# Optimization experiments

Hardware: AMD Instinct MI355X
Metric: run time of the kernel (lower is better)

The kernel has to match this reference:

```python
import jax, jax.numpy as jnp
import numpy as np

DEGREE = 3
NUM_POINTS = 1024
EPS = 1e-5


def jacobi_kan(x, coeffs, a=1.0, b=1.0, degree=DEGREE):
    # x: (B, C_in, N) -> y: (B, C_out, N)
    t = jnp.tanh(jnp.transpose(x, (0, 2, 1)))  # (B, N, C_in)
    polys = [jnp.ones_like(t)]
    if degree > 0:
        polys.append((a - b + (a + b + 2.0) * t) / 2.0)
    for i in range(2, degree + 1):
        A = (2 * i + a + b - 1) * (2 * i + a + b) / (2 * i * (i + a + b))
        B = (2 * i + a + b - 1) * (a ** 2 - b ** 2) / (2 * i * (i + a + b) * (2 * i + a + b - 2))
        C = -2 * (i + a - 1) * (i + b - 1) * (2 * i + a + b) / (2 * i * (i + a + b) * (2 * i + a + b - 2))
        polys.append((A * t + B) * polys[-1] + C * polys[-2])
    jac = jnp.stack(polys, axis=-1)  # (B, N, C_in, D+1)
    return jnp.einsum('bnid,iod->bon', jac, coeffs)


def batchnorm(x):
    # x: (B, C, N); training-mode BN with batch stats, gamma=1, beta=0
    m = jnp.mean(x, axis=(0, 2), keepdims=True)
    v = jnp.var(x, axis=(0, 2), keepdims=True)
    return (x - m) * jax.lax.rsqrt(v + EPS)


def setup_inputs() -> dict:
    key = jax.random.key(0)
    ks = jax.random.split(key, 11)
    dims = [(2, 64), (64, 64), (64, 64), (64, 128), (128, 1024),
            (1088, 512), (512, 256), (256, 128), (128, 128), (128, 3)]
    inp = {"x": jax.random.normal(ks[0], (32, 2, NUM_POINTS), dtype=jnp.float32)}
    for idx, (i, o) in enumerate(dims):
        std = 1.0 / (i * (DEGREE + 1))
        inp[f"w{idx+1}"] = std * jax.random.normal(ks[idx + 1], (i, o, DEGREE + 1), dtype=jnp.float32)
    return inp


def reference(x, w1, w2, w3, w4, w5, w6, w7, w8, w9, w10):
    h = batchnorm(jacobi_kan(x, w1))
    h = batchnorm(jacobi_kan(h, w2))
    local_feature = h                                  # (B, 64, N)
    h = batchnorm(jacobi_kan(h, w3))
    h = batchnorm(jacobi_kan(h, w4))
    h = batchnorm(jacobi_kan(h, w5))                   # (B, 1024, N)
    gf = jnp.max(h, axis=2, keepdims=True)             # (B, 1024, 1)
    gf = jnp.broadcast_to(gf, (h.shape[0], h.shape[1], NUM_POINTS))
    h = jnp.concatenate([local_feature, gf], axis=1)   # (B, 1088, N)
    h = batchnorm(jacobi_kan(h, w6))
    h = batchnorm(jacobi_kan(h, w7))
    h = batchnorm(jacobi_kan(h, w8))
    h = batchnorm(jacobi_kan(h, w9))
    return jacobi_kan(h, w10)                          # (B, 3, N)
```

## Files before the change

kernel.cpp:

```cpp
#include <hip/hip_runtime.h>

#define BATCH 32
#define NPTS  1024
#define NTOT  (BATCH * NPTS)

typedef _Float16 half8  __attribute__((ext_vector_type(8)));
typedef _Float16 half2v __attribute__((ext_vector_type(2)));
typedef float    f32x4  __attribute__((ext_vector_type(4)));


__device__ __forceinline__ float fast_tanh(float x) {
  float ax = fabsf(x);
  float e  = __expf(-2.0f * ax);
  float t  = (1.0f - e) / (1.0f + e);
  return x < 0.0f ? -t : t;
}

__device__ __forceinline__ void jacobi4(float t, float& p0, float& p1, float& p2, float& p3) {
  float t2 = t * t;
  p0 = 1.0f;
  p1 = 2.0f * t;
  p2 = 3.75f * t2 - 0.75f;
  p3 = t * (7.0f * t2 - 3.0f);
}

__device__ __forceinline__ unsigned encf(float f) {
  unsigned b = __float_as_uint(f);
  return b ^ ((unsigned)((int)b >> 31) | 0x80000000u);
}
__device__ __forceinline__ float decf(unsigned u) {
  unsigned b = (u & 0x80000000u) ? (u ^ 0x80000000u) : ~u;
  return __uint_as_float(b);
}

__global__ void zero_ws(unsigned* __restrict__ p, int n) {
  int i = blockIdx.x * 256 + threadIdx.x;
  if (i < n) p[i] = 0u;
}

__global__ void conv_w16(const float* __restrict__ w, half8* __restrict__ wh,
                         int C_in, int C_out, int BN) {
  const int nslot = C_in >> 1;
  int tid = blockIdx.x * 256 + threadIdx.x;
  int oL = tid % BN;
  int r  = tid / BN;
  int s  = r % nslot;
  int ot = r / nslot;
  int i  = s << 1;
  int o  = ot * BN + oL;
  const float4 wa = *(const float4*)(w + (((size_t)i * C_out + o) << 2));
  const float4 wb = *(const float4*)(w + (((size_t)(i + 1) * C_out + o) << 2));
  half8 h;
  h[0] = (_Float16)(wa.x * 64.0f); h[1] = (_Float16)(wa.y * 64.0f);
  h[2] = (_Float16)(wa.z * 64.0f); h[3] = (_Float16)(wa.w * 64.0f);
  h[4] = (_Float16)(wb.x * 64.0f); h[5] = (_Float16)(wb.y * 64.0f);
  h[6] = (_Float16)(wb.z * 64.0f); h[7] = (_Float16)(wb.w * 64.0f);
  wh[tid] = h;
}

__global__ __launch_bounds__(256) void act_tanh16(
    const float* __restrict__ y, const float2* __restrict__ st,
    unsigned* __restrict__ T16, int C)
{
  const int nslot = C >> 1;
  const int b  = blockIdx.x / nslot;
  const int s  = blockIdx.x - b * nslot;
  const int n  = threadIdx.x << 2;
  const float* yp = y + (((size_t)(b * C + (s << 1))) << 10) + n;
  const float2 s0 = st[(s << 1)];
  const float2 s1 = st[(s << 1) + 1];
  float4 v0 = *(const float4*)yp;
  float4 v1 = *(const float4*)(yp + 1024);
  float a0[4] = {v0.x, v0.y, v0.z, v0.w};
  float a1[4] = {v1.x, v1.y, v1.z, v1.w};
  unsigned r[4];
#pragma unroll
  for (int k = 0; k < 4; ++k) {
    _Float16 h0 = (_Float16)fast_tanh((a0[k] - s0.x) * s0.y);
    _Float16 h1 = (_Float16)fast_tanh((a1[k] - s1.x) * s1.y);
    unsigned lo = (unsigned)__builtin_bit_cast(unsigned short, h0);
    unsigned hi = (unsigned)__builtin_bit_cast(unsigned short, h1);
    r[k] = lo | (hi << 16);
  }
  *(uint4*)(T16 + (((size_t)(b * nslot + s)) << 10) + n) = make_uint4(r[0], r[1], r[2], r[3]);
}

template<int NBW>
__global__ __launch_bounds__(NBW * 128, 2) void kan_mfma7(
    const unsigned* __restrict__ T16,
    const half8* __restrict__ wh,
    const float* __restrict__ bias,
    float*       __restrict__ out,
    float2*      __restrict__ spart,
    float*       __restrict__ stat_acc,
    unsigned*    __restrict__ max_acc,
    int C_in, int C_out)
{
  constexpr int BN = NBW * 64;
  const int nslot = C_in >> 1;
  __shared__ float sredS[BN][2], sredS2[BN][2], sredM[BN][2];

  const int t    = threadIdx.x;
  const int lane = t & 63;
  const int col  = lane & 15;
  const int quad = lane >> 4;
  const int wv   = t >> 6;
  const int wm   = wv & 1;
  const int wn   = wv >> 1;
  const int b    = blockIdx.x >> 3;
  const int n0   = (blockIdx.x & 7) << 7;
  const int o0   = blockIdx.y * BN;

  f32x4 acc[4][4];
#pragma unroll
  for (int i = 0; i < 4; ++i)
#pragma unroll
    for (int j = 0; j < 4; ++j)
#pragma unroll
      for (int k = 0; k < 4; ++k) acc[i][j][k] = 0.0f;

  const unsigned* Tp = T16 + (((size_t)(b * nslot + quad)) << 10) + n0 + (wm << 6) + col;
  const half8*    Bp = wh + (size_t)blockIdx.y * nslot * BN + (size_t)quad * BN + wn * 64 + col;

  const half2v c375  = {(_Float16)3.75f,  (_Float16)3.75f};
  const half2v cm075 = {(_Float16)-0.75f, (_Float16)-0.75f};
  const half2v c70   = {(_Float16)7.0f,   (_Float16)7.0f};
  const half2v cm30  = {(_Float16)-3.0f,  (_Float16)-3.0f};

#define KLOAD(TTR, BFR, J) do {                                            \
    const unsigned* tp_ = Tp + (((size_t)(unsigned)(J)) << 12);            \
    const half8*    bp_ = Bp + (size_t)(unsigned)(J) * (BN << 2);          \
    TTR[0] = tp_[0];  TTR[1] = tp_[16];                                    \
    TTR[2] = tp_[32]; TTR[3] = tp_[48];                                    \
    BFR[0] = bp_[0];  BFR[1] = bp_[16];                                    \
    BFR[2] = bp_[32]; BFR[3] = bp_[48];                                    \
  } while (0)

#define KSTEP(TTR, BFR) do {                                               \
    half8 af_[4];                                                          \
    _Pragma("unroll")                                                      \
    for (int fm_ = 0; fm_ < 4; ++fm_) {                                    \
      half2v tt = __builtin_bit_cast(half2v, TTR[fm_]);                    \
      half2v t2 = tt * tt;                                                 \
      half2v q1 = tt + tt;                                                 \
      half2v q2 = t2 * c375 + cm075;                                       \
      half2v q3 = tt * (t2 * c70 + cm30);                                  \
      half8 h;                                                             \
      h[0] = (_Float16)1.0f; h[1] = q1[0]; h[2] = q2[0]; h[3] = q3[0];     \
      h[4] = (_Float16)1.0f; h[5] = q1[1]; h[6] = q2[1]; h[7] = q3[1];     \
      af_[fm_] = h;                                                        \
    }                                                                      \
    _Pragma("unroll")                                                      \
    for (int fm_ = 0; fm_ < 4; ++fm_) {                                    \
      _Pragma("unroll")                                                    \
      for (int fn_ = 0; fn_ < 4; ++fn_)                                    \
        acc[fm_][fn_] = __builtin_amdgcn_mfma_f32_16x16x32_f16(            \
            af_[fm_], BFR[fn_], acc[fm_][fn_], 0, 0, 0);                   \
    }                                                                      \
  } while (0)

  const int nIt = nslot >> 2;
  unsigned ttA[4], ttB[4];
  half8    bfA[4], bfB[4];
  KLOAD(ttA, bfA, 0);
  KLOAD(ttB, bfB, 1);
  int it = 0;
  for (; it + 3 < nIt; it += 2) {
    KSTEP(ttA, bfA); KLOAD(ttA, bfA, it + 2);
    KSTEP(ttB, bfB); KLOAD(ttB, bfB, it + 3);
  }
  KSTEP(ttA, bfA);
  KSTEP(ttB, bfB);

#undef KLOAD
#undef KSTEP

  const float inv64 = 0.015625f;
#pragma unroll
  for (int fn = 0; fn < 4; ++fn) {
    const int cl = (wn << 6) + (fn << 4) + col;
    const int o  = o0 + cl;
    const float bb = bias ? bias[b * C_out + o] : 0.0f;
    float s = 0.f, s2 = 0.f, mx = -3.4e38f;
#pragma unroll
    for (int fm = 0; fm < 4; ++fm) {
      float v0 = acc[fm][fn][0] * inv64 + bb;
      float v1 = acc[fm][fn][1] * inv64 + bb;
      float v2 = acc[fm][fn][2] * inv64 + bb;
      float v3 = acc[fm][fn][3] * inv64 + bb;
      if (out) {
        *(float4*)(out + (((size_t)(b * C_out + o)) << 10) + n0 + (wm << 6) + (fm << 4) + (quad << 2)) =
            make_float4(v0, v1, v2, v3);
      }
      s  += v0 + v1 + v2 + v3;
      s2 += v0 * v0 + v1 * v1 + v2 * v2 + v3 * v3;
      mx  = fmaxf(fmaxf(v0, v1), fmaxf(fmaxf(v2, v3), mx));
    }
    s  += __shfl_down(s, 32);  s  += __shfl_down(s, 16);
    s2 += __shfl_down(s2, 32); s2 += __shfl_down(s2, 16);
    mx  = fmaxf(mx, __shfl_down(mx, 32)); mx = fmaxf(mx, __shfl_down(mx, 16));
    if (lane < 16) {
      sredS [cl][wm] = s;
      sredS2[cl][wm] = s2;
      sredM [cl][wm] = mx;
    }
  }
  __syncthreads();
  if (t < BN) {
    const int o = o0 + t;
    float s  = sredS [t][0] + sredS [t][1];
    float s2 = sredS2[t][0] + sredS2[t][1];
    if (out) {
      spart[(o << 8) + blockIdx.x] = make_float2(s, s2);
    } else {
      float mx = fmaxf(sredM[t][0], sredM[t][1]);
      atomicAdd(&stat_acc[o], s);
      atomicAdd(&stat_acc[C_out + o], s2);
      atomicMax(&max_acc[b * C_out + o], encf(mx));
    }
  }
}

template<int BM, int BN>
__global__ __launch_bounds__(256) void kan_gemm(
    const float*  __restrict__ in, const float2* __restrict__ stats,
    const float*  __restrict__ w, float* __restrict__ out,
    float2* __restrict__ spart, int C_in, int C_out)
{
  static_assert(BM * BN == 256 * 64, "8x8-per-thread tile requires BM*BN == 16384");
  constexpr int TM = BM / 8;
  constexpr int AE = 8 * BM / 256;
  constexpr int BE = 8 * BN / 256;
  __shared__ __align__(16) float As[32][BM];
  __shared__ __align__(16) float Bs[32][BN];

  const int t  = threadIdx.x;
  const int tpb = NPTS / BM;
  const int b  = blockIdx.x / tpb;
  const int n0 = (blockIdx.x % tpb) * BM;
  const int o0 = blockIdx.y * BN;
  const int tm = t % TM;
  const int to = t / TM;

  float acc[2][4][2][4];
#pragma unroll
  for (int a = 0; a < 2; ++a)
#pragma unroll
    for (int c = 0; c < 4; ++c)
#pragma unroll
      for (int d = 0; d < 2; ++d)
#pragma unroll
        for (int e = 0; e < 4; ++e) acc[a][c][d][e] = 0.0f;

  const int nch = (C_in + 7) >> 3;
  for (int ch = 0; ch < nch; ++ch) {
    const int i0 = ch << 3;
    __syncthreads();
#pragma unroll
    for (int r = 0; r < AE; ++r) {
      int e  = t + (r << 8);
      int il = e / BM, n = e % BM;
      int i  = i0 + il;
      float p0 = 0.f, p1 = 0.f, p2 = 0.f, p3 = 0.f;
      if (i < C_in) {
        float v = in[((size_t)(b * C_in + i) << 10) + n0 + n];
        if (stats) { float2 s = stats[i]; v = (v - s.x) * s.y; }
        jacobi4(fast_tanh(v), p0, p1, p2, p3);
      }
      As[(il << 2) + 0][n] = p0;
      As[(il << 2) + 1][n] = p1;
      As[(il << 2) + 2][n] = p2;
      As[(il << 2) + 3][n] = p3;
    }
#pragma unroll
    for (int r = 0; r < BE; ++r) {
      int e  = t + (r << 8);
      int il = e / BN, o = e % BN;
      int i  = i0 + il;
      float4 wv = make_float4(0.f, 0.f, 0.f, 0.f);
      if (i < C_in) wv = *(const float4*)(w + (((size_t)i * C_out + o0 + o) << 2));
      Bs[(il << 2) + 0][o] = wv.x;
      Bs[(il << 2) + 1][o] = wv.y;
      Bs[(il << 2) + 2][o] = wv.z;
      Bs[(il << 2) + 3][o] = wv.w;
    }
    __syncthreads();
#pragma unroll 8
    for (int k = 0; k < 32; ++k) {
      const float4 a0 = *(const float4*)&As[k][tm << 2];
      const float4 a1 = *(const float4*)&As[k][(BM / 2) + (tm << 2)];
      const float4 b0 = *(const float4*)&Bs[k][to << 2];
      const float4 b1 = *(const float4*)&Bs[k][(BN / 2) + (to << 2)];
      const float am[2][4] = {{a0.x, a0.y, a0.z, a0.w}, {a1.x, a1.y, a1.z, a1.w}};
      const float bo[2][4] = {{b0.x, b0.y, b0.z, b0.w}, {b1.x, b1.y, b1.z, b1.w}};
#pragma unroll
      for (int oh = 0; oh < 2; ++oh)
#pragma unroll
        for (int oj = 0; oj < 4; ++oj) {
          const float bv = bo[oh][oj];
#pragma unroll
          for (int mh = 0; mh < 2; ++mh)
#pragma unroll
            for (int mj = 0; mj < 4; ++mj)
              acc[oh][oj][mh][mj] = fmaf(bv, am[mh][mj], acc[oh][oj][mh][mj]);
        }
    }
  }

#pragma unroll
  for (int oh = 0; oh < 2; ++oh)
#pragma unroll
    for (int oj = 0; oj < 4; ++oj) {
      const int o = o0 + oh * (BN / 2) + (to << 2) + oj;
      float s = 0.f, s2 = 0.f;
#pragma unroll
      for (int mh = 0; mh < 2; ++mh) {
        float4 v = make_float4(acc[oh][oj][mh][0], acc[oh][oj][mh][1],
                               acc[oh][oj][mh][2], acc[oh][oj][mh][3]);
        *(float4*)(out + (((size_t)(b * C_out + o)) << 10) + n0 + mh * (BM / 2) + (tm << 2)) = v;
        s  += v.x + v.y + v.z + v.w;
        s2 += v.x * v.x + v.y * v.y + v.z * v.z + v.w * v.w;
      }
#pragma unroll
      for (int off = TM / 2; off > 0; off >>= 1) {
        s  += __shfl_down(s, off, TM);
        s2 += __shfl_down(s2, off, TM);
      }
      if (tm == 0) spart[(o << 8) + blockIdx.x] = make_float2(s, s2);
    }
}

__global__ __launch_bounds__(256) void bn_finalize2(
    const float2* __restrict__ spart, float2* __restrict__ stats, int C, int nxb)
{
  int c = blockIdx.x, t = threadIdx.x;
  float s = 0.f, s2 = 0.f;
  if (t < nxb) { float2 p = spart[(c << 8) + t]; s = p.x; s2 = p.y; }
#pragma unroll
  for (int off = 32; off > 0; off >>= 1) {
    s  += __shfl_down(s, off);
    s2 += __shfl_down(s2, off);
  }
  __shared__ float rs[4], rs2[4];
  int wid = t >> 6;
  if ((t & 63) == 0) { rs[wid] = s; rs2[wid] = s2; }
  __syncthreads();
  if (t == 0) {
    s  = rs[0] + rs[1] + rs[2] + rs[3];
    s2 = rs2[0] + rs2[1] + rs2[2] + rs2[3];
    float m   = s * (1.0f / NTOT);
    float var = s2 * (1.0f / NTOT) - m * m;
    stats[c] = make_float2(m, rsqrtf(var + 1e-5f));
  }
}

__global__ void bn_finalize(const float* __restrict__ stat_acc,
                            float2* __restrict__ stats, int C) {
  int c = blockIdx.x * 256 + threadIdx.x;
  if (c < C) {
    float m   = stat_acc[c] * (1.0f / NTOT);
    float var = stat_acc[C + c] * (1.0f / NTOT) - m * m;
    stats[c] = make_float2(m, rsqrtf(var + 1e-5f));
  }
}

__global__ __launch_bounds__(256) void pool_const6p(
    const unsigned* __restrict__ max_acc, const float2* __restrict__ stats5,
    const float* __restrict__ w6, float* __restrict__ cst)
{
  __shared__ __align__(16) float4 P[32][64];
  const int t  = threadIdx.x;
  const int ot = blockIdx.x;
  const int c0 = blockIdx.y << 6;
#pragma unroll
  for (int it = 0; it < 8; ++it) {
    int idx = t + (it << 8);
    int b = idx >> 6, cl = idx & 63;
    int c = c0 + cl;
    float mx = decf(max_acc[(b << 10) + c]);
    float2 s = stats5[c];
    float tt = fast_tanh((mx - s.x) * s.y);
    float p0, p1, p2, p3; jacobi4(tt, p0, p1, p2, p3);
    P[b][cl] = make_float4(p0, p1, p2, p3);
  }
  __syncthreads();
  const int oL = t & 63;
  const int bg = t >> 6;
  const int o  = (ot << 6) + oL;
  float acc[8];
#pragma unroll
  for (int i = 0; i < 8; ++i) acc[i] = 0.f;
  for (int cl = 0; cl < 64; ++cl) {
    const float4 wv = *(const float4*)(w6 + (((size_t)(64 + c0 + cl) * 512 + o) << 2));
#pragma unroll
    for (int bb = 0; bb < 8; ++bb) {
      float4 p = P[(bg << 3) + bb][cl];
      acc[bb] += p.x * wv.x + p.y * wv.y + p.z * wv.z + p.w * wv.w;
    }
  }
#pragma unroll
  for (int bb = 0; bb < 8; ++bb)
    atomicAdd(&cst[(((bg << 3) + bb) << 9) + o], acc[bb]);
}

__global__ __launch_bounds__(256) void kan_final(
    const float* __restrict__ in, const float2* __restrict__ stats,
    const float* __restrict__ w, float* __restrict__ out)
{
  int g = blockIdx.x * 256 + threadIdx.x;
  int b = g >> 10, n = g & 1023;
  float a0 = 0.f, a1 = 0.f, a2 = 0.f;
  for (int i = 0; i < 128; ++i) {
    float v = in[((size_t)(b * 128 + i) << 10) + n];
    float2 s = stats[i];
    float p0, p1, p2, p3; jacobi4(fast_tanh((v - s.x) * s.y), p0, p1, p2, p3);
    const float4 w0 = *(const float4*)(w + ((i * 3 + 0) << 2));
    const float4 w1 = *(const float4*)(w + ((i * 3 + 1) << 2));
    const float4 w2 = *(const float4*)(w + ((i * 3 + 2) << 2));
    a0 += p0 * w0.x + p1 * w0.y + p2 * w0.z + p3 * w0.w;
    a1 += p0 * w1.x + p1 * w1.y + p2 * w1.z + p3 * w1.w;
    a2 += p0 * w2.x + p1 * w2.y + p2 * w2.z + p3 * w2.w;
  }
  out[((b * 3 + 0) << 10) + n] = a0;
  out[((b * 3 + 1) << 10) + n] = a1;
  out[((b * 3 + 2) << 10) + n] = a2;
}

extern "C" void kernel_launch(void* const* d_in, const int* in_sizes, int n_in,
                              void* d_out, int out_size, void* d_ws, size_t ws_size,
                              hipStream_t stream) {
  const float* x   = (const float*)d_in[0];
  const float* w1  = (const float*)d_in[1];
  const float* w2  = (const float*)d_in[2];
  const float* w3  = (const float*)d_in[3];
  const float* w4  = (const float*)d_in[4];
  const float* w5  = (const float*)d_in[5];
  const float* w6  = (const float*)d_in[6];
  const float* w7  = (const float*)d_in[7];
  const float* w8  = (const float*)d_in[8];
  const float* w9  = (const float*)d_in[9];
  const float* w10 = (const float*)d_in[10];

  float* ws = (float*)d_ws;
  float*    stat_acc = ws + 0;
  unsigned* maxenc   = (unsigned*)(ws + 2048);
  float*    cst6     = ws + 34816;
  float2*   spart    = (float2*)(ws + 51200);
  float2*   stats1   = (float2*)(ws + 313344);
  float2*   stats2   = stats1 + 64;
  float2*   stats3   = stats2 + 64;
  float2*   stats4   = stats3 + 64;
  float2*   stats5   = stats4 + 128;
  float2*   stats6   = stats5 + 1024;
  float2*   stats7   = stats6 + 512;
  float2*   stats8   = stats7 + 256;
  float2*   stats9   = stats8 + 128;
  half8*    whbase = (half8*)(ws + 318464);
  half8*    h2 = whbase + 0;
  half8*    h3 = whbase + 2048;
  half8*    h4 = whbase + 4096;
  half8*    h5 = whbase + 8192;
  half8*    h6 = whbase + 73728;
  half8*    h7 = whbase + 90112;
  half8*    h8 = whbase + 155648;
  half8*    h9 = whbase + 172032;
  const size_t MF = 1048576;
  float*    P   = ws + MF;
  unsigned* T2  = (unsigned*)(P + 0 * MF);
  float*    y1  = P + 1 * MF;
  unsigned* T1  = (unsigned*)(P + 3 * MF);
  float*    y2  = P + 1 * MF;
  float*    y3  = P + 1 * MF;
  unsigned* T3  = (unsigned*)(P + 3 * MF);
  float*    y4  = P + 4 * MF;
  unsigned* T4  = (unsigned*)(P + 1 * MF);
  float*    y6  = P + 3 * MF;
  unsigned* T6  = (unsigned*)(P + 19 * MF);
  float*    y7  = P + 0 * MF;
  unsigned* T7  = (unsigned*)(P + 8 * MF);
  float*    y8  = P + 0 * MF;
  unsigned* T8  = (unsigned*)(P + 4 * MF);
  float*    y9  = P + 12 * MF;

  dim3 blk(256);
  zero_ws<<<200, blk, 0, stream>>>((unsigned*)ws, 51200);
  conv_w16<<<8,   blk, 0, stream>>>(w2, h2, 64, 64, 64);
  conv_w16<<<8,   blk, 0, stream>>>(w3, h3, 64, 64, 64);
  conv_w16<<<16,  blk, 0, stream>>>(w4, h4, 64, 128, 128);
  conv_w16<<<256, blk, 0, stream>>>(w5, h5, 128, 1024, 128);
  conv_w16<<<64,  blk, 0, stream>>>(w6, h6, 64, 512, 128);
  conv_w16<<<256, blk, 0, stream>>>(w7, h7, 512, 256, 128);
  conv_w16<<<64,  blk, 0, stream>>>(w8, h8, 256, 128, 128);
  conv_w16<<<32,  blk, 0, stream>>>(w9, h9, 128, 128, 128);

  kan_gemm<256, 64><<<dim3(128, 1), blk, 0, stream>>>(x, nullptr, w1, y1, spart, 2, 64);
  bn_finalize2<<<64, blk, 0, stream>>>(spart, stats1, 64, 128);
  act_tanh16<<<32 * 32, blk, 0, stream>>>(y1, stats1, T1, 64);
  kan_mfma7<1><<<dim3(256, 1), 128, 0, stream>>>(T1, h2, nullptr, y2, spart, nullptr, nullptr, 64, 64);
  bn_finalize2<<<64, blk, 0, stream>>>(spart, stats2, 64, 256);
  act_tanh16<<<32 * 32, blk, 0, stream>>>(y2, stats2, T2, 64);
  kan_mfma7<1><<<dim3(256, 1), 128, 0, stream>>>(T2, h3, nullptr, y3, spart, nullptr, nullptr, 64, 64);
  bn_finalize2<<<64, blk, 0, stream>>>(spart, stats3, 64, 256);
  act_tanh16<<<32 * 32, blk, 0, stream>>>(y3, stats3, T3, 64);
  kan_mfma7<2><<<dim3(256, 1), blk, 0, stream>>>(T3, h4, nullptr, y4, spart, nullptr, nullptr, 64, 128);
  bn_finalize2<<<128, blk, 0, stream>>>(spart, stats4, 128, 256);
  act_tanh16<<<32 * 64, blk, 0, stream>>>(y4, stats4, T4, 128);
  kan_mfma7<2><<<dim3(256, 8), blk, 0, stream>>>(T4, h5, nullptr, nullptr, nullptr, stat_acc, maxenc, 128, 1024);
  bn_finalize<<<4, blk, 0, stream>>>(stat_acc, stats5, 1024);
  pool_const6p<<<dim3(8, 16), blk, 0, stream>>>(maxenc, stats5, w6, cst6);
  kan_mfma7<2><<<dim3(256, 4), blk, 0, stream>>>(T2, h6, cst6, y6, spart, nullptr, nullptr, 64, 512);
  bn_finalize2<<<512, blk, 0, stream>>>(spart, stats6, 512, 256);
  act_tanh16<<<32 * 256, blk, 0, stream>>>(y6, stats6, T6, 512);
  kan_mfma7<2><<<dim3(256, 2), blk, 0, stream>>>(T6, h7, nullptr, y7, spart, nullptr, nullptr, 512, 256);
  bn_finalize2<<<256, blk, 0, stream>>>(spart, stats7, 256, 256);
  act_tanh16<<<32 * 128, blk, 0, stream>>>(y7, stats7, T7, 256);
  kan_mfma7<2><<<dim3(256, 1), blk, 0, stream>>>(T7, h8, nullptr, y8, spart, nullptr, nullptr, 256, 128);
  bn_finalize2<<<128, blk, 0, stream>>>(spart, stats8, 128, 256);
  act_tanh16<<<32 * 64, blk, 0, stream>>>(y8, stats8, T8, 128);
  kan_mfma7<2><<<dim3(256, 1), blk, 0, stream>>>(T8, h9, nullptr, y9, spart, nullptr, nullptr, 128, 128);
  bn_finalize2<<<128, blk, 0, stream>>>(spart, stats9, 128, 256);
  kan_final<<<128, blk, 0, stream>>>(y9, stats9, w10, (float*)d_out);
}
```

Baseline: 382.6 us.

## Drop constant P0 term from MFMA K dimension via precomputed weight row sums

Because the degree-0 Jacobi polynomial is always 1, its contribution is a per-output-channel sum of weights. The change precomputes that sum in a new kernel and adds it as a bias in the epilogue, so the MFMA loop only multiplies the three non-constant polynomial terms. Weights are repacked by degree (P1, P2, P3 groups of 8 input channels), which shrinks the GEMM K dimension by a quarter. In exchange the kernel holds more registers (16 T values and 12 B fragments per stage, double-buffered), which may cut occupancy, and it adds eight small launches.

```diff
diff --git a/kernel.cpp b/kernel.cpp
--- a/kernel.cpp
+++ b/kernel.cpp
@@ -38,24 +38,43 @@
   if (i < n) p[i] = 0u;
 }
 
-__global__ void conv_w16(const float* __restrict__ w, half8* __restrict__ wh,
-                         int C_in, int C_out, int BN) {
-  const int nslot = C_in >> 1;
+__global__ __launch_bounds__(256) void conv_w16p(
+    const float* __restrict__ w, half8* __restrict__ wh,
+    int C_in, int C_out, int BN)
+{
+  const int NS = C_in >> 5;
   int tid = blockIdx.x * 256 + threadIdx.x;
   int oL = tid % BN;
   int r  = tid / BN;
-  int s  = r % nslot;
-  int ot = r / nslot;
-  int i  = s << 1;
+  int pr = NS * 12;
+  int ot = r / pr;
+  int r2 = r - ot * pr;
+  int q  = r2 & 3;
+  int jj = (r2 >> 2) % 3;
+  int s  = (r2 >> 2) / 3;
   int o  = ot * BN + oL;
-  const float4 wa = *(const float4*)(w + (((size_t)i * C_out + o) << 2));
-  const float4 wb = *(const float4*)(w + (((size_t)(i + 1) * C_out + o) << 2));
+  int cb = (s << 5) + (q << 3);
   half8 h;
-  h[0] = (_Float16)(wa.x * 64.0f); h[1] = (_Float16)(wa.y * 64.0f);
-  h[2] = (_Float16)(wa.z * 64.0f); h[3] = (_Float16)(wa.w * 64.0f);
-  h[4] = (_Float16)(wb.x * 64.0f); h[5] = (_Float16)(wb.y * 64.0f);
-  h[6] = (_Float16)(wb.z * 64.0f); h[7] = (_Float16)(wb.w * 64.0f);
+#pragma unroll
+  for (int e = 0; e < 8; ++e) {
+    float v = w[(((size_t)(cb + e) * C_out + o) << 2) + (jj + 1)];
+    h[e] = (_Float16)(v * 64.0f);
+  }
   wh[tid] = h;
+}
+
+__global__ __launch_bounds__(256) void w0sum(
+    const float* __restrict__ w, float* __restrict__ s, int C_in, int C_out)
+{
+  __shared__ float r[3][64];
+  const int oL  = threadIdx.x & 63;
+  const int seg = threadIdx.x >> 6;
+  const int o   = (blockIdx.x << 6) + oL;
+  float a = 0.f;
+  for (int i = seg; i < C_in; i += 4) a += w[(((size_t)i * C_out + o) << 2)];
+  if (seg) r[seg - 1][oL] = a;
+  __syncthreads();
+  if (seg == 0) s[o] = a + r[0][oL] + r[1][oL] + r[2][oL];
 }
 
 __global__ __launch_bounds__(256) void act_tanh16(
@@ -86,9 +105,10 @@
 }
 
 template<int NBW>
-__global__ __launch_bounds__(NBW * 128, 2) void kan_mfma7(
+__global__ __launch_bounds__(NBW * 128, 2) void kan_mfma8(
     const unsigned* __restrict__ T16,
     const half8* __restrict__ wh,
+    const float* __restrict__ w0s,
     const float* __restrict__ bias,
     float*       __restrict__ out,
     float2*      __restrict__ spart,
@@ -98,6 +118,7 @@
 {
   constexpr int BN = NBW * 64;
   const int nslot = C_in >> 1;
+  const int NS    = C_in >> 5;
   __shared__ float sredS[BN][2], sredS2[BN][2], sredM[BN][2];
 
   const int t    = threadIdx.x;
@@ -119,53 +140,100 @@
 #pragma unroll
       for (int k = 0; k < 4; ++k) acc[i][j][k] = 0.0f;
 
-  const unsigned* Tp = T16 + (((size_t)(b * nslot + quad)) << 10) + n0 + (wm << 6) + col;
-  const half8*    Bp = wh + (size_t)blockIdx.y * nslot * BN + (size_t)quad * BN + wn * 64 + col;
+  const unsigned* Tp = T16 + (((size_t)(b * nslot + (quad << 2))) << 10) + n0 + (wm << 6) + col;
+  const half8*    Bp = wh + ((size_t)blockIdx.y * NS * 12 + quad) * BN + wn * 64 + col;
 
   const half2v c375  = {(_Float16)3.75f,  (_Float16)3.75f};
   const half2v cm075 = {(_Float16)-0.75f, (_Float16)-0.75f};
   const half2v c70   = {(_Float16)7.0f,   (_Float16)7.0f};
   const half2v cm30  = {(_Float16)-3.0f,  (_Float16)-3.0f};
 
-#define KLOAD(TTR, BFR, J) do {                                            \
-    const unsigned* tp_ = Tp + (((size_t)(unsigned)(J)) << 12);            \
-    const half8*    bp_ = Bp + (size_t)(unsigned)(J) * (BN << 2);          \
-    TTR[0] = tp_[0];  TTR[1] = tp_[16];                                    \
-    TTR[2] = tp_[32]; TTR[3] = tp_[48];                                    \
-    BFR[0] = bp_[0];  BFR[1] = bp_[16];                                    \
-    BFR[2] = bp_[32]; BFR[3] = bp_[48];                                    \
-  } while (0)
-
-#define KSTEP(TTR, BFR) do {                                               \
-    half8 af_[4];                                                          \
+#define KLOAD(TT, BF, S) do {                                              \
     _Pragma("unroll")                                                      \
-    for (int fm_ = 0; fm_ < 4; ++fm_) {                                    \
-      half2v tt = __builtin_bit_cast(half2v, TTR[fm_]);                    \
-      half2v t2 = tt * tt;                                                 \
-      half2v q1 = tt + tt;                                                 \
-      half2v q2 = t2 * c375 + cm075;                                       \
-      half2v q3 = tt * (t2 * c70 + cm30);                                  \
-      half8 h;                                                             \
-      h[0] = (_Float16)1.0f; h[1] = q1[0]; h[2] = q2[0]; h[3] = q3[0];     \
-      h[4] = (_Float16)1.0f; h[5] = q1[1]; h[6] = q2[1]; h[7] = q3[1];     \
-      af_[fm_] = h;                                                        \
+    for (int f_ = 0; f_ < 4; ++f_) {                                       \
+      _Pragma("unroll")                                                    \
+      for (int r_ = 0; r_ < 4; ++r_)                                       \
+        TT[f_ * 4 + r_] = Tp[(((size_t)(unsigned)((S) * 16 + r_)) << 10) + (f_ << 4)]; \
     }                                                                      \
     _Pragma("unroll")                                                      \
-    for (int fm_ = 0; fm_ < 4; ++fm_) {                                    \
+    for (int j_ = 0; j_ < 3; ++j_) {                                       \
       _Pragma("unroll")                                                    \
       for (int fn_ = 0; fn_ < 4; ++fn_)                                    \
-        acc[fm_][fn_] = __builtin_amdgcn_mfma_f32_16x16x32_f16(            \
-            af_[fm_], BFR[fn_], acc[fm_][fn_], 0, 0, 0);                   \
+        BF[j_ * 4 + fn_] = Bp[(size_t)(unsigned)((S) * 12 + j_ * 4) * BN + (fn_ << 4)]; \
     }                                                                      \
   } while (0)
 
-  const int nIt = nslot >> 2;
-  unsigned ttA[4], ttB[4];
-  half8    bfA[4], bfB[4];
+#define KSTEP(TT, BF) do {                                                 \
+    {                                                \
+      half8 ap_[4];                                                        \
+      _Pragma("unroll")                                                    \
+      for (int f_ = 0; f_ < 4; ++f_) {                                     \
+        unsigned u_[4];                                                    \
+        _Pragma("unroll")                                                  \
+        for (int r_ = 0; r_ < 4; ++r_) {                                   \
+          half2v tt = __builtin_bit_cast(half2v, TT[f_ * 4 + r_]);         \
+          u_[r_] = __builtin_bit_cast(unsigned, (half2v)(tt + tt));        \
+        }                                                                  \
+        ap_[f_] = __builtin_bit_cast(half8, make_uint4(u_[0], u_[1], u_[2], u_[3])); \
+      }                                                                    \
+      _Pragma("unroll")                                                    \
+      for (int fm_ = 0; fm_ < 4; ++fm_) {                                  \
+        _Pragma("unroll")                                                  \
+        for (int fn_ = 0; fn_ < 4; ++fn_)                                  \
+          acc[fm_][fn_] = __builtin_amdgcn_mfma_f32_16x16x32_f16(          \
+              ap_[fm_], BF[fn_], acc[fm_][fn_], 0, 0, 0);                  \
+      }                                                                    \
+    }                                                                      \
+    {                                    \
+      half8 ap_[4];                                                        \
+      _Pragma("unroll")                                                    \
+      for (int f_ = 0; f_ < 4; ++f_) {                                     \
+        unsigned u_[4];                                                    \
+        _Pragma("unroll")                                                  \
+        for (int r_ = 0; r_ < 4; ++r_) {                                   \
+          half2v tt = __builtin_bit_cast(half2v, TT[f_ * 4 + r_]);         \
+          half2v t2 = tt * tt;                                             \
+          u_[r_] = __builtin_bit_cast(unsigned, (half2v)(t2 * c375 + cm075)); \
+        }                                                                  \
+        ap_[f_] = __builtin_bit_cast(half8, make_uint4(u_[0], u_[1], u_[2], u_[3])); \
+      }                                                                    \
+      _Pragma("unroll")                                                    \
+      for (int fm_ = 0; fm_ < 4; ++fm_) {                                  \
+        _Pragma("unroll")                                                  \
+        for (int fn_ = 0; fn_ < 4; ++fn_)                                  \
+          acc[fm_][fn_] = __builtin_amdgcn_mfma_f32_16x16x32_f16(          \
+              ap_[fm_], BF[4 + fn_], acc[fm_][fn_], 0, 0, 0);              \
+      }                                                                    \
+    }                                                                      \
+    {                                       \
+      half8 ap_[4];                                                        \
+      _Pragma("unroll")                                                    \
+      for (int f_ = 0; f_ < 4; ++f_) {                                     \
+        unsigned u_[4];                                                    \
+        _Pragma("unroll")                                                  \
+        for (int r_ = 0; r_ < 4; ++r_) {                                   \
+          half2v tt = __builtin_bit_cast(half2v, TT[f_ * 4 + r_]);         \
+          half2v t2 = tt * tt;                                             \
+          u_[r_] = __builtin_bit_cast(unsigned, (half2v)(tt * (t2 * c70 + cm30))); \
+        }                                                                  \
+        ap_[f_] = __builtin_bit_cast(half8, make_uint4(u_[0], u_[1], u_[2], u_[3])); \
+      }                                                                    \
+      _Pragma("unroll")                                                    \
+      for (int fm_ = 0; fm_ < 4; ++fm_) {                                  \
+        _Pragma("unroll")                                                  \
+        for (int fn_ = 0; fn_ < 4; ++fn_)                                  \
+          acc[fm_][fn_] = __builtin_amdgcn_mfma_f32_16x16x32_f16(          \
+              ap_[fm_], BF[8 + fn_], acc[fm_][fn_], 0, 0, 0);              \
+      }                                                                    \
+    }                                                                      \
+  } while (0)
+
+  unsigned ttA[16], ttB[16];
+  half8    bfA[12], bfB[12];
   KLOAD(ttA, bfA, 0);
   KLOAD(ttB, bfB, 1);
   int it = 0;
-  for (; it + 3 < nIt; it += 2) {
+  for (; it + 3 < NS; it += 2) {
     KSTEP(ttA, bfA); KLOAD(ttA, bfA, it + 2);
     KSTEP(ttB, bfB); KLOAD(ttB, bfB, it + 3);
   }
@@ -180,7 +248,7 @@
   for (int fn = 0; fn < 4; ++fn) {
     const int cl = (wn << 6) + (fn << 4) + col;
     const int o  = o0 + cl;
-    const float bb = bias ? bias[b * C_out + o] : 0.0f;
+    const float bb = w0s[o] + (bias ? bias[b * C_out + o] : 0.0f);
     float s = 0.f, s2 = 0.f, mx = -3.4e38f;
 #pragma unroll
     for (int fm = 0; fm < 4; ++fm) {
@@ -455,15 +523,23 @@
   float2*   stats7   = stats6 + 512;
   float2*   stats8   = stats7 + 256;
   float2*   stats9   = stats8 + 128;
-  half8*    whbase = (half8*)(ws + 318464);
-  half8*    h2 = whbase + 0;
-  half8*    h3 = whbase + 2048;
-  half8*    h4 = whbase + 4096;
-  half8*    h5 = whbase + 8192;
-  half8*    h6 = whbase + 73728;
-  half8*    h7 = whbase + 90112;
-  half8*    h8 = whbase + 155648;
-  half8*    h9 = whbase + 172032;
+  float*    w0s2 = ws + 318080;
+  float*    w0s3 = w0s2 + 64;
+  float*    w0s4 = w0s3 + 64;
+  float*    w0s5 = w0s4 + 128;
+  float*    w0s6 = w0s5 + 1024;
+  float*    w0s7 = w0s6 + 512;
+  float*    w0s8 = w0s7 + 256;
+  float*    w0s9 = w0s8 + 128;
+  half8*    whb = (half8*)(ws + 320384);
+  half8*    h2 = whb + 0;
+  half8*    h3 = whb + 1536;
+  half8*    h4 = whb + 3072;
+  half8*    h5 = whb + 6144;
+  half8*    h6 = whb + 55296;
+  half8*    h7 = whb + 67584;
+  half8*    h8 = whb + 116736;
+  half8*    h9 = whb + 129024;
   const size_t MF = 1048576;
   float*    P   = ws + MF;
   unsigned* T2  = (unsigned*)(P + 0 * MF);
@@ -484,40 +560,48 @@
 
   dim3 blk(256);
   zero_ws<<<200, blk, 0, stream>>>((unsigned*)ws, 51200);
-  conv_w16<<<8,   blk, 0, stream>>>(w2, h2, 64, 64, 64);
-  conv_w16<<<8,   blk, 0, stream>>>(w3, h3, 64, 64, 64);
-  conv_w16<<<16,  blk, 0, stream>>>(w4, h4, 64, 128, 128);
-  conv_w16<<<256, blk, 0, stream>>>(w5, h5, 128, 1024, 128);
-  conv_w16<<<64,  blk, 0, stream>>>(w6, h6, 64, 512, 128);
-  conv_w16<<<256, blk, 0, stream>>>(w7, h7, 512, 256, 128);
-  conv_w16<<<64,  blk, 0, stream>>>(w8, h8, 256, 128, 128);
-  conv_w16<<<32,  blk, 0, stream>>>(w9, h9, 128, 128, 128);
+  conv_w16p<<<6,   blk, 0, stream>>>(w2, h2, 64, 64, 64);
+  conv_w16p<<<6,   blk, 0, stream>>>(w3, h3, 64, 64, 64);
+  conv_w16p<<<12,  blk, 0, stream>>>(w4, h4, 64, 128, 128);
+  conv_w16p<<<192, blk, 0, stream>>>(w5, h5, 128, 1024, 128);
+  conv_w16p<<<48,  blk, 0, stream>>>(w6, h6, 64, 512, 128);
+  conv_w16p<<<192, blk, 0, stream>>>(w7, h7, 512, 256, 128);
+  conv_w16p<<<48,  blk, 0, stream>>>(w8, h8, 256, 128, 128);
+  conv_w16p<<<24,  blk, 0, stream>>>(w9, h9, 128, 128, 128);
+  w0sum<<<1,  blk, 0, stream>>>(w2, w0s2, 64, 64);
+  w0sum<<<1,  blk, 0, stream>>>(w3, w0s3, 64, 64);
+  w0sum<<<2,  blk, 0, stream>>>(w4, w0s4, 64, 128);
+  w0sum<<<16, blk, 0, stream>>>(w5, w0s5, 128, 1024);
+  w0sum<<<8,  blk, 0, stream>>>(w6, w0s6, 64, 512);
+  w0sum<<<4,  blk, 0, stream>>>(w7, w0s7, 512, 256);
+  w0sum<<<2,  blk, 0, stream>>>(w8, w0s8, 256, 128);
+  w0sum<<<2,  blk, 0, stream>>>(w9, w0s9, 128, 128);
 
   kan_gemm<256, 64><<<dim3(128, 1), blk, 0, stream>>>(x, nullptr, w1, y1, spart, 2, 64);
   bn_finalize2<<<64, blk, 0, stream>>>(spart, stats1, 64, 128);
   act_tanh16<<<32 * 32, blk, 0, stream>>>(y1, stats1, T1, 64);
-  kan_mfma7<1><<<dim3(256, 1), 128, 0, stream>>>(T1, h2, nullptr, y2, spart, nullptr, nullptr, 64, 64);
+  kan_mfma8<1><<<dim3(256, 1), 128, 0, stream>>>(T1, h2, w0s2, nullptr, y2, spart, nullptr, nullptr, 64, 64);
   bn_finalize2<<<64, blk, 0, stream>>>(spart, stats2, 64, 256);
   act_tanh16<<<32 * 32, blk, 0, stream>>>(y2, stats2, T2, 64);
-  kan_mfma7<1><<<dim3(256, 1), 128, 0, stream>>>(T2, h3, nullptr, y3, spart, nullptr, nullptr, 64, 64);
+  kan_mfma8<1><<<dim3(256, 1), 128, 0, stream>>>(T2, h3, w0s3, nullptr, y3, spart, nullptr, nullptr, 64, 64);
   bn_finalize2<<<64, blk, 0, stream>>>(spart, stats3, 64, 256);
   act_tanh16<<<32 * 32, blk, 0, stream>>>(y3, stats3, T3, 64);
-  kan_mfma7<2><<<dim3(256, 1), blk, 0, stream>>>(T3, h4, nullptr, y4, spart, nullptr, nullptr, 64, 128);
+  kan_mfma8<2><<<dim3(256, 1), blk, 0, stream>>>(T3, h4, w0s4, nullptr, y4, spart, nullptr, nullptr, 64, 128);
   bn_finalize2<<<128, blk, 0, stream>>>(spart, stats4, 128, 256);
   act_tanh16<<<32 * 64, blk, 0, stream>>>(y4, stats4, T4, 128);
-  kan_mfma7<2><<<dim3(256, 8), blk, 0, stream>>>(T4, h5, nullptr, nullptr, nullptr, stat_acc, maxenc, 128, 1024);
+  kan_mfma8<2><<<dim3(256, 8), blk, 0, stream>>>(T4, h5, w0s5, nullptr, nullptr, nullptr, stat_acc, maxenc, 128, 1024);
   bn_finalize<<<4, blk, 0, stream>>>(stat_acc, stats5, 1024);
   pool_const6p<<<dim3(8, 16), blk, 0, stream>>>(maxenc, stats5, w6, cst6);
-  kan_mfma7<2><<<dim3(256, 4), blk, 0, stream>>>(T2, h6, cst6, y6, spart, nullptr, nullptr, 64, 512);
+  kan_mfma8<2><<<dim3(256, 4), blk, 0, stream>>>(T2, h6, w0s6, cst6, y6, spart, nullptr, nullptr, 64, 512);
   bn_finalize2<<<512, blk, 0, stream>>>(spart, stats6, 512, 256);
   act_tanh16<<<32 * 256, blk, 0, stream>>>(y6, stats6, T6, 512);
-  kan_mfma7<2><<<dim3(256, 2), blk, 0, stream>>>(T6, h7, nullptr, y7, spart, nullptr, nullptr, 512, 256);
+  kan_mfma8<2><<<dim3(256, 2), blk, 0, stream>>>(T6, h7, w0s7, nullptr, y7, spart, nullptr, nullptr, 512, 256);
   bn_finalize2<<<256, blk, 0, stream>>>(spart, stats7, 256, 256);
   act_tanh16<<<32 * 128, blk, 0, stream>>>(y7, stats7, T7, 256);
-  kan_mfma7<2><<<dim3(256, 1), blk, 0, stream>>>(T7, h8, nullptr, y8, spart, nullptr, nullptr, 256, 128);
+  kan_mfma8<2><<<dim3(256, 1), blk, 0, stream>>>(T7, h8, w0s8, nullptr, y8, spart, nullptr, nullptr, 256, 128);
   bn_finalize2<<<128, blk, 0, stream>>>(spart, stats8, 128, 256);
   act_tanh16<<<32 * 64, blk, 0, stream>>>(y8, stats8, T8, 128);
-  kan_mfma7<2><<<dim3(256, 1), blk, 0, stream>>>(T8, h9, nullptr, y9, spart, nullptr, nullptr, 128, 128);
+  kan_mfma8<2><<<dim3(256, 1), blk, 0, stream>>>(T8, h9, w0s9, nullptr, y9, spart, nullptr, nullptr, 128, 128);
   bn_finalize2<<<128, blk, 0, stream>>>(spart, stats9, 128, 256);
   kan_final<<<128, blk, 0, stream>>>(y9, stats9, w10, (float*)d_out);
 }
```

Result: slower. 439.8 us (+14.9%).
